# Kernel tuning notes

Measured on AMD Instinct MI355X. Metric: run time of the kernel, lower is better.

## Reference

```python
import jax, jax.numpy as jnp
import numpy as np

N = 65536        # number of encoding vectors (flattened tokens)
K = 1024         # num_embeddings (codebook size)
D = 128          # embedding_dim
BETA = 0.25


def setup_inputs() -> dict:
    key = jax.random.key(0)
    k_enc, k_cb = jax.random.split(key)
    encoding = jax.random.normal(k_enc, (N, D), dtype=jnp.float32)
    # nn.Embedding weight initialized uniform(-1/K, 1/K)
    codebook = jax.random.uniform(k_cb, (K, D), dtype=jnp.float32,
                                  minval=-1.0 / K, maxval=1.0 / K)
    return {"encoding": encoding, "codebook": codebook}


def reference(encoding, codebook):
    # Nearest codebook entry per row. argmin of L2 distance == argmin of
    # squared distance; expand ||e - w||^2 = ||e||^2 - 2 e.w + ||w||^2.
    # ||e||^2 is constant per row, so it does not affect the argmin.
    scores = (-2.0 * jnp.einsum('nd,kd->nk', encoding, codebook)
              + jnp.sum(codebook * codebook, axis=-1)[None, :])  # [N, K]
    quantized_index = jnp.argmin(scores, axis=-1)                # [N] int
    quantized_embedding = codebook[quantized_index]              # [N, D] gather == onehot @ W

    sg = jax.lax.stop_gradient
    commitment_loss = jnp.mean((sg(quantized_embedding) - encoding) ** 2)
    embedding_loss = jnp.mean((quantized_embedding - sg(encoding)) ** 2)
    vq_loss = commitment_loss * BETA + embedding_loss

    # straight-through estimator
    quantized_st = encoding + sg(quantized_embedding - encoding)

    quantized_index = quantized_index[:, None]  # match torch unsqueeze(1) -> [N, 1]
    return (quantized_index, quantized_st, vq_loss, embedding_loss, commitment_loss)
```

## Files before the change

### kernel.cpp

```cpp
#include <hip/hip_runtime.h>


#define NROWS 65536
#define KCB   1024
#define DIM   128
#define DV    32
#define MSE_DENOM 8388608.0f
#define MARGIN 3.0e-5f
#define FLAGCAP 16384
#define CSCALE   1024.0f
#define CDESCALE 0.0009765625f

#define WS_CNORM_F  256
#define WS_CN1024_F 1280
#define WS_LIST_B   12288
#define WS_PH_B     77824
#define WS_NEEDED   339968

typedef __attribute__((ext_vector_type(16))) float float16v;
typedef _Float16 half8 __attribute__((ext_vector_type(8)));
union U4H8 { uint4 u; half8 h; };
union F4A  { float4 v; float f[4]; };
union F16V { float16v v; float f[16]; };
union HU   { _Float16 f; unsigned short u; };

__device__ __forceinline__ float fmed3(float a, float b, float c) {
  return __builtin_amdgcn_fmed3f(a, b, c);
}

__global__ __launch_bounds__(64) void vq_prep0(const float* __restrict__ C,
                                               float* __restrict__ wsf) {
  int k = blockIdx.x * 64 + threadIdx.x;
  if (k == 0) { wsf[0] = 0.0f; ((unsigned*)wsf)[1] = 0u; }
  const float4* c4 = (const float4*)C + (size_t)k * DV;
  float s = 0.f;
#pragma unroll 8
  for (int i = 0; i < DV; ++i) {
    float4 v = c4[i];
    s = fmaf(v.x, v.x, s); s = fmaf(v.y, v.y, s);
    s = fmaf(v.z, v.z, s); s = fmaf(v.w, v.w, s);
  }
  wsf[WS_CNORM_F + k]  = s;
  wsf[WS_CN1024_F + k] = s * CSCALE;
}

__global__ __launch_bounds__(256) void vq_pack(const float* __restrict__ C,
                                               uint4* __restrict__ PH) {
  int g = blockIdx.x * 256 + threadIdx.x;
  int mt = g >> 9, s = (g >> 6) & 7, l = g & 63;
  int cw = mt * 32 + (l & 31);
  int k0 = s * 16 + (l >> 5) * 8;
  const float* src = C + (size_t)cw * DIM + k0;
  float4 x0 = *(const float4*)src;
  float4 x1 = *(const float4*)(src + 4);
  unsigned h[8];
  {
    float v[8] = {x0.x, x0.y, x0.z, x0.w, x1.x, x1.y, x1.z, x1.w};
#pragma unroll
    for (int j = 0; j < 8; ++j) { HU u; u.f = (_Float16)(CSCALE * v[j]); h[j] = u.u; }
  }
  PH[g] = make_uint4(h[0] | (h[1] << 16), h[2] | (h[3] << 16),
                     h[4] | (h[5] << 16), h[6] | (h[7] << 16));
}

__global__ __launch_bounds__(512, 1) void vq_main7(const float* __restrict__ E,
                                                   const float* __restrict__ C,
                                                   float* __restrict__ wsf,
                                                   float* __restrict__ out) {
  __shared__ uint4 SB[2][4096];
  __shared__ __align__(16) float CN[1024];
  __shared__ int BI[256];

  const int tid  = threadIdx.x;
  const int w    = tid >> 6;
  const int l    = tid & 63;
  const int half = l >> 5;
  const int rr   = l & 31;
  const int row0 = blockIdx.x * 256;

  const uint4* PHg = (const uint4*)((const char*)wsf + WS_PH_B);
  const uint4* CNg = (const uint4*)(wsf + WS_CN1024_F);

  uint4 stg[8];
#pragma unroll
  for (int j = 0; j < 8; ++j) stg[j] = PHg[j * 512 + tid];
  uint4 cnr;
  if (tid < 256) cnr = CNg[tid];

  half8 beh[8];
  float s2 = 0.f;
  const float* erow = E + (size_t)(row0 + w * 32 + rr) * DIM + half * 8;
#pragma unroll
  for (int s = 0; s < 8; ++s) {
    float4 x0 = *(const float4*)(erow + s * 16);
    float4 x1 = *(const float4*)(erow + s * 16 + 4);
    float v[8] = {x0.x, x0.y, x0.z, x0.w, x1.x, x1.y, x1.z, x1.w};
#pragma unroll
    for (int j = 0; j < 8; ++j) {
      float y = v[j];
      s2 = fmaf(y, y, s2);
      beh[s][j] = (_Float16)(-2.f * y);
    }
  }

#pragma unroll
  for (int j = 0; j < 8; ++j) SB[0][j * 512 + tid] = stg[j];
  if (tid < 256) ((uint4*)CN)[tid] = cnr;
  __syncthreads();

  float m1 = 3.0e38f, m2 = 3.0e38f;
  int bi0 = 0;

  for (int qt = 0; qt < 4; ++qt) {
    const int b = qt & 1;
    if (qt < 3) {
#pragma unroll
      for (int j = 0; j < 8; ++j) stg[j] = PHg[(qt + 1) * 4096 + j * 512 + tid];
    }
    const int kq = qt * 256;

#pragma unroll
    for (int tt = 0; tt < 8; ++tt) {
      const int tg = qt * 8 + tt;
      U4H8 h[8];
#pragma unroll
      for (int s = 0; s < 8; ++s) h[s].u = SB[b][tt * 512 + s * 64 + l];
      F16V acc;
#pragma unroll
      for (int q = 0; q < 4; ++q) {
        F4A c; c.v = *(const float4*)&CN[tg * 32 + q * 8 + half * 4];
        acc.f[q * 4 + 0] = c.f[0]; acc.f[q * 4 + 1] = c.f[1];
        acc.f[q * 4 + 2] = c.f[2]; acc.f[q * 4 + 3] = c.f[3];
      }
#pragma unroll
      for (int s = 0; s < 8; ++s)
        acc.v = __builtin_amdgcn_mfma_f32_32x32x16_f16(h[s].h, beh[s], acc.v, 0, 0, 0);
#pragma unroll
      for (int reg = 0; reg < 16; ++reg) {
        float sc = acc.f[reg] * CDESCALE;
        m2 = fmed3(sc, m1, m2);
        if (sc < m1) bi0 = kq + tt * 32 + (reg >> 2) * 8 + (reg & 3);
        m1 = fminf(m1, sc);
      }
    }

    if (qt < 3) {
#pragma unroll
      for (int j = 0; j < 8; ++j) SB[b ^ 1][j * 512 + tid] = stg[j];
    }
    __syncthreads();
  }

  int   bi  = bi0 + half * 4;
  float obm  = __shfl_xor(m1, 32, 64);
  float obm2 = __shfl_xor(m2, 32, 64);
  int   obi  = __shfl_xor(bi, 32, 64);
  float oen  = __shfl_xor(s2, 32, 64);
  float sv = fminf(fminf(m2, obm2), fmaxf(m1, obm));
  float bv; int bif;
  if (obm < m1 || (obm == m1 && obi < bi)) { bv = obm; bif = obi; }
  else                                     { bv = m1;  bif = bi;  }
  float en = s2 + oen;

  if (half == 0) {
    const int r = w * 32 + rr;
    out[row0 + r] = (float)bif;
    BI[r] = bif;
    if (sv - bv < MARGIN) {
      unsigned idx = atomicAdd((unsigned*)wsf + 1, 1u);
      if (idx < FLAGCAP) ((int*)((char*)wsf + WS_LIST_B))[idx] = row0 + r;
    }
    float term = en + bv;
#pragma unroll
    for (int off = 16; off > 0; off >>= 1) term += __shfl_down(term, off);
    if (rr == 0) atomicAdd(wsf, term);
  }
  __syncthreads();

  const float4* C4   = (const float4*)C;
  float4*       out4 = (float4*)out;
#pragma unroll
  for (int it = 0; it < 16; ++it) {
    int flat = it * 512 + tid;
    int r = flat >> 5, d4 = flat & 31;
    out4[(NROWS / 4) + (size_t)(row0 + r) * DV + d4] = C4[(size_t)BI[r] * DV + d4];
  }
}

__global__ __launch_bounds__(256) void vq_fix(const float* __restrict__ E,
                                              const float* __restrict__ C,
                                              float* __restrict__ wsf,
                                              float* __restrict__ out) {
  __shared__ float4 eL[4][32];
  __shared__ float  RV[4][4];
  __shared__ int    RI[4][4];
  __shared__ int    RESi[4];
  const int tid = threadIdx.x;
  const int wv  = tid >> 6;
  const int ln  = tid & 63;
  const int* list = (const int*)((const char*)wsf + WS_LIST_B);
  int nf = (int)((const unsigned*)wsf)[1];
  if (nf > FLAGCAP) nf = FLAGCAP;
  const float4* E4 = (const float4*)E;
  const float4* C4 = (const float4*)C;
  const float*  cn = wsf + WS_CNORM_F;
  float4* out4 = (float4*)out;

  for (int g = blockIdx.x; g * 4 < nf; g += gridDim.x) {
    const int base = g * 4;
    if (tid < 128) {
      int r = tid >> 5, d4 = tid & 31;
      int R = (base + r < nf) ? list[base + r] : list[base];
      eL[r][d4] = E4[(size_t)R * DV + d4];
    }
    __syncthreads();
    float bv[4] = {3.0e38f, 3.0e38f, 3.0e38f, 3.0e38f};
    int   bi[4] = {0, 0, 0, 0};
#pragma unroll
    for (int j = 0; j < 4; ++j) {
      int k = j * 256 + tid;
      float d0 = 0.f, d1 = 0.f, d2 = 0.f, d3 = 0.f;
#pragma unroll 4
      for (int d4 = 0; d4 < 32; ++d4) {
        float4 c = C4[(size_t)k * DV + d4];
        float4 e0 = eL[0][d4], e1 = eL[1][d4], e2 = eL[2][d4], e3 = eL[3][d4];
        d0 = fmaf(c.x, e0.x, d0); d0 = fmaf(c.y, e0.y, d0);
        d0 = fmaf(c.z, e0.z, d0); d0 = fmaf(c.w, e0.w, d0);
        d1 = fmaf(c.x, e1.x, d1); d1 = fmaf(c.y, e1.y, d1);
        d1 = fmaf(c.z, e1.z, d1); d1 = fmaf(c.w, e1.w, d1);
        d2 = fmaf(c.x, e2.x, d2); d2 = fmaf(c.y, e2.y, d2);
        d2 = fmaf(c.z, e2.z, d2); d2 = fmaf(c.w, e2.w, d2);
        d3 = fmaf(c.x, e3.x, d3); d3 = fmaf(c.y, e3.y, d3);
        d3 = fmaf(c.z, e3.z, d3); d3 = fmaf(c.w, e3.w, d3);
      }
      float cnk = cn[k];
      float s0 = fmaf(-2.f, d0, cnk);
      float s1 = fmaf(-2.f, d1, cnk);
      float s2 = fmaf(-2.f, d2, cnk);
      float s3 = fmaf(-2.f, d3, cnk);
      if (s0 < bv[0] || (s0 == bv[0] && k < bi[0])) { bv[0] = s0; bi[0] = k; }
      if (s1 < bv[1] || (s1 == bv[1] && k < bi[1])) { bv[1] = s1; bi[1] = k; }
      if (s2 < bv[2] || (s2 == bv[2] && k < bi[2])) { bv[2] = s2; bi[2] = k; }
      if (s3 < bv[3] || (s3 == bv[3] && k < bi[3])) { bv[3] = s3; bi[3] = k; }
    }
#pragma unroll
    for (int off = 32; off > 0; off >>= 1) {
#pragma unroll
      for (int r = 0; r < 4; ++r) {
        float wv_ = __shfl_down(bv[r], off);
        int   ji  = __shfl_down(bi[r], off);
        if (wv_ < bv[r] || (wv_ == bv[r] && ji < bi[r])) { bv[r] = wv_; bi[r] = ji; }
      }
    }
    if (ln == 0) {
#pragma unroll
      for (int r = 0; r < 4; ++r) { RV[wv][r] = bv[r]; RI[wv][r] = bi[r]; }
    }
    __syncthreads();
    if (tid < 4) {
      float v = RV[0][tid]; int i = RI[0][tid];
#pragma unroll
      for (int q = 1; q < 4; ++q) {
        float vv = RV[q][tid]; int ii = RI[q][tid];
        if (vv < v || (vv == v && ii < i)) { v = vv; i = ii; }
      }
      RESi[tid] = i;
      if (base + tid < nf) out[list[base + tid]] = (float)i;
    }
    __syncthreads();
    if (tid < 128) {
      int r = tid >> 5, d4 = tid & 31;
      if (base + r < nf) {
        int R = list[base + r];
        out4[(NROWS / 4) + (size_t)R * DV + d4] = C4[(size_t)RESi[r] * DV + d4];
      }
    }
    __syncthreads();
  }
}

__global__ void vq_final(const float* __restrict__ wsf, float* __restrict__ out) {
  if (threadIdx.x == 0 && blockIdx.x == 0) {
    float mse = wsf[0] / MSE_DENOM;
    out[NROWS + NROWS * DIM + 0] = 1.25f * mse;
    out[NROWS + NROWS * DIM + 1] = mse;
    out[NROWS + NROWS * DIM + 2] = mse;
  }
}

__global__ __launch_bounds__(256) void vq_prep_fb(const float* __restrict__ C,
                                                  float* __restrict__ ws) {
  int k = blockIdx.x * 256 + threadIdx.x;
  if (k == 0) ws[0] = 0.0f;
  const float4* c4 = (const float4*)C + (size_t)k * DV;
  float s = 0.f;
#pragma unroll 8
  for (int i = 0; i < DV; ++i) {
    float4 v = c4[i];
    s = fmaf(v.x, v.x, s); s = fmaf(v.y, v.y, s);
    s = fmaf(v.z, v.z, s); s = fmaf(v.w, v.w, s);
  }
  ws[64 + k] = s;
}

__global__ __launch_bounds__(256) void vq_main_fb(const float* __restrict__ E,
                                                  const float* __restrict__ C,
                                                  const float* __restrict__ cnorm,
                                                  float* __restrict__ out,
                                                  float* __restrict__ lossacc) {
  __shared__ float smem[16384];
  float4* EsV = (float4*)smem;
  float4* CsV = (float4*)(smem + 8192);
  const int tid  = threadIdx.x;
  const int row0 = blockIdx.x * 64;
#pragma unroll
  for (int i = 0; i < 8; ++i) {
    int flat = i * 256 + tid;
    int r = flat >> 5, d4 = flat & 31;
    EsV[r * 32 + (d4 ^ (r & 31))] = ((const float4*)E)[(size_t)(row0 + r) * DV + d4];
  }
  const int tx = tid & 15, ty = tid >> 4;
  int rbase[4], rmask[4];
#pragma unroll
  for (int i = 0; i < 4; ++i) { int r = i * 16 + ty; rbase[i] = r * 32; rmask[i] = r & 31; }
  float bestv[4]; int besti[4];
#pragma unroll
  for (int i = 0; i < 4; ++i) { bestv[i] = 3.0e38f; besti[i] = 0; }
  for (int ch = 0; ch < 16; ++ch) {
    const int k0 = ch * 64;
    __syncthreads();
#pragma unroll
    for (int i = 0; i < 8; ++i) {
      int flat = i * 256 + tid;
      int k = flat >> 5, d4 = flat & 31;
      CsV[k * 32 + (d4 ^ (k & 31))] = ((const float4*)C)[(size_t)(k0 + k) * DV + d4];
    }
    __syncthreads();
    float acc[4][4] = {};
#pragma unroll 8
    for (int d4 = 0; d4 < DV; ++d4) {
      float4 a[4], b[4];
#pragma unroll
      for (int i = 0; i < 4; ++i) a[i] = EsV[rbase[i] + (d4 ^ rmask[i])];
#pragma unroll
      for (int j = 0; j < 4; ++j) { int k = j * 16 + tx; b[j] = CsV[k * 32 + (d4 ^ (k & 31))]; }
#pragma unroll
      for (int i = 0; i < 4; ++i)
#pragma unroll
        for (int j = 0; j < 4; ++j) {
          acc[i][j] = fmaf(a[i].x, b[j].x, acc[i][j]);
          acc[i][j] = fmaf(a[i].y, b[j].y, acc[i][j]);
          acc[i][j] = fmaf(a[i].z, b[j].z, acc[i][j]);
          acc[i][j] = fmaf(a[i].w, b[j].w, acc[i][j]);
        }
    }
#pragma unroll
    for (int j = 0; j < 4; ++j) {
      int kg = k0 + j * 16 + tx;
      float cnv = cnorm[kg];
#pragma unroll
      for (int i = 0; i < 4; ++i) {
        float s = fmaf(-2.0f, acc[i][j], cnv);
        if (s < bestv[i] || (s == bestv[i] && kg < besti[i])) { bestv[i] = s; besti[i] = kg; }
      }
    }
  }
  float* Rv = smem + 8192;
  int*   Ri = (int*)(smem + 9216);
  int*   BIf = (int*)(smem + 10240);
  __syncthreads();
#pragma unroll
  for (int i = 0; i < 4; ++i) {
    int r = i * 16 + ty;
    Rv[r * 16 + tx] = bestv[i];
    Ri[r * 16 + tx] = besti[i];
  }
  __syncthreads();
  if (tid < 64) {
    const int r = tid;
    float bv = Rv[r * 16]; int bi = Ri[r * 16];
#pragma unroll
    for (int t = 1; t < 16; ++t) {
      float v = Rv[r * 16 + t]; int ii = Ri[r * 16 + t];
      if (v < bv || (v == bv && ii < bi)) { bv = v; bi = ii; }
    }
    float en = 0.f;
#pragma unroll 8
    for (int d4 = 0; d4 < DV; ++d4) {
      float4 v = EsV[r * 32 + (d4 ^ (r & 31))];
      en = fmaf(v.x, v.x, en); en = fmaf(v.y, v.y, en);
      en = fmaf(v.z, v.z, en); en = fmaf(v.w, v.w, en);
    }
    out[row0 + r] = (float)bi;
    BIf[r] = bi;
    float blocksum = en + bv;
#pragma unroll
    for (int off = 32; off > 0; off >>= 1) blocksum += __shfl_down(blocksum, off);
    if (tid == 0) atomicAdd(lossacc, blocksum);
  }
  __syncthreads();
  const float4* C4   = (const float4*)C;
  float4*       out4 = (float4*)out;
  for (int flat = tid; flat < 64 * DV; flat += 256) {
    int r = flat >> 5, d4 = flat & 31;
    out4[(NROWS / 4) + (size_t)(row0 + r) * DV + d4] = C4[(size_t)BIf[r] * DV + d4];
  }
}

__global__ void vq_final_fb(const float* __restrict__ ws, float* __restrict__ out) {
  if (threadIdx.x == 0 && blockIdx.x == 0) {
    float mse = ws[0] / MSE_DENOM;
    out[NROWS + NROWS * DIM + 0] = 1.25f * mse;
    out[NROWS + NROWS * DIM + 1] = mse;
    out[NROWS + NROWS * DIM + 2] = mse;
  }
}

extern "C" void kernel_launch(void* const* d_in, const int* in_sizes, int n_in,
                              void* d_out, int out_size, void* d_ws, size_t ws_size,
                              hipStream_t stream) {
  const float* E = (const float*)d_in[0];
  const float* C = (const float*)d_in[1];
  float* out = (float*)d_out;
  float* wsf = (float*)d_ws;

  if (ws_size >= (size_t)WS_NEEDED) {
    uint4* PH = (uint4*)((char*)d_ws + WS_PH_B);
    vq_prep0<<<16, 64, 0, stream>>>(C, wsf);
    vq_pack<<<64, 256, 0, stream>>>(C, PH);
    vq_main7<<<NROWS / 256, 512, 0, stream>>>(E, C, wsf, out);
    vq_fix<<<256, 256, 0, stream>>>(E, C, wsf, out);
    vq_final<<<1, 64, 0, stream>>>(wsf, out);
  } else {
    vq_prep_fb<<<4, 256, 0, stream>>>(C, wsf);
    vq_main_fb<<<NROWS / 64, 256, 0, stream>>>(E, C, wsf + 64, out, wsf);
    vq_final_fb<<<1, 64, 0, stream>>>(wsf, out);
  }
}
```

Before: 178.6 us.

## Split codebook across wave pairs with smaller blocks and async LDS loads

Replaces the 512-thread, 256-row main kernel with a 256-thread, 64-row kernel in which two wave pairs each scan half of the codebook, then merge their min, second-min and index through shared memory. Codebook tiles are streamed straight into LDS with global_load_lds double buffering instead of being staged in registers. Each tile's MFMA chain is split across two accumulators to shorten the dependency chain, and the descale multiply moves out of the inner loop, with the margin rescaled to match. The smaller LDS footprint allows several blocks per CU for better latency hiding, at the cost of more blocks each reloading the codebook and a larger fix-up grid.

```diff
diff --git a/kernel.cpp b/kernel.cpp
--- a/kernel.cpp
+++ b/kernel.cpp
@@ -7,6 +7,7 @@
 #define DV    32
 #define MSE_DENOM 8388608.0f
 #define MARGIN 3.0e-5f
+#define MARGINS 0.030720f
 #define FLAGCAP 16384
 #define CSCALE   1024.0f
 #define CDESCALE 0.0009765625f
@@ -26,6 +27,11 @@
 
 __device__ __forceinline__ float fmed3(float a, float b, float c) {
   return __builtin_amdgcn_fmed3f(a, b, c);
+}
+__device__ __forceinline__ void gload16(const void* g, void* s) {
+  __builtin_amdgcn_global_load_lds((const __attribute__((address_space(1))) unsigned int*)g,
+                                   (__attribute__((address_space(3))) unsigned int*)s,
+                                   16, 0, 0);
 }
 
 __global__ __launch_bounds__(64) void vq_prep0(const float* __restrict__ C,
@@ -63,33 +69,40 @@
                      h[4] | (h[5] << 16), h[6] | (h[7] << 16));
 }
 
-__global__ __launch_bounds__(512, 1) void vq_main7(const float* __restrict__ E,
+__global__ __launch_bounds__(256, 4) void vq_main8(const float* __restrict__ E,
                                                    const float* __restrict__ C,
                                                    float* __restrict__ wsf,
                                                    float* __restrict__ out) {
-  __shared__ uint4 SB[2][4096];
+  __shared__ uint4 SH[2][1024];
   __shared__ __align__(16) float CN[1024];
-  __shared__ int BI[256];
+  __shared__ float X1[64], X2[64];
+  __shared__ int   XI[64];
+  __shared__ int   BI[64];
 
   const int tid  = threadIdx.x;
   const int w    = tid >> 6;
   const int l    = tid & 63;
   const int half = l >> 5;
   const int rr   = l & 31;
-  const int row0 = blockIdx.x * 256;
+  const int pair = w >> 1;
+  const int rw   = w & 1;
+  const int row0 = blockIdx.x * 64;
+  const int row  = row0 + rw * 32 + rr;
 
   const uint4* PHg = (const uint4*)((const char*)wsf + WS_PH_B);
-  const uint4* CNg = (const uint4*)(wsf + WS_CN1024_F);
-
-  uint4 stg[8];
-#pragma unroll
-  for (int j = 0; j < 8; ++j) stg[j] = PHg[j * 512 + tid];
-  uint4 cnr;
-  if (tid < 256) cnr = CNg[tid];
+
+  {
+    uint4* base = &SH[0][0];
+    gload16(PHg + tid,                  base + tid);
+    gload16(PHg + 256 + tid,            base + 256 + tid);
+    gload16(PHg + 16 * 512 + tid,       base + 512 + tid);
+    gload16(PHg + 16 * 512 + 256 + tid, base + 768 + tid);
+    gload16(((const uint4*)(wsf + WS_CN1024_F)) + tid, ((uint4*)CN) + tid);
+  }
 
   half8 beh[8];
   float s2 = 0.f;
-  const float* erow = E + (size_t)(row0 + w * 32 + rr) * DIM + half * 8;
+  const float* erow = E + (size_t)row * DIM + half * 8;
 #pragma unroll
   for (int s = 0; s < 8; ++s) {
     float4 x0 = *(const float4*)(erow + s * 16);
@@ -103,74 +116,84 @@
     }
   }
 
-#pragma unroll
-  for (int j = 0; j < 8; ++j) SB[0][j * 512 + tid] = stg[j];
-  if (tid < 256) ((uint4*)CN)[tid] = cnr;
+  asm volatile("s_waitcnt vmcnt(0)" ::: "memory");
   __syncthreads();
 
   float m1 = 3.0e38f, m2 = 3.0e38f;
-  int bi0 = 0;
-
-  for (int qt = 0; qt < 4; ++qt) {
-    const int b = qt & 1;
-    if (qt < 3) {
-#pragma unroll
-      for (int j = 0; j < 8; ++j) stg[j] = PHg[(qt + 1) * 4096 + j * 512 + tid];
-    }
-    const int kq = qt * 256;
-
-#pragma unroll
-    for (int tt = 0; tt < 8; ++tt) {
-      const int tg = qt * 8 + tt;
-      U4H8 h[8];
-#pragma unroll
-      for (int s = 0; s < 8; ++s) h[s].u = SB[b][tt * 512 + s * 64 + l];
-      F16V acc;
-#pragma unroll
-      for (int q = 0; q < 4; ++q) {
-        F4A c; c.v = *(const float4*)&CN[tg * 32 + q * 8 + half * 4];
-        acc.f[q * 4 + 0] = c.f[0]; acc.f[q * 4 + 1] = c.f[1];
-        acc.f[q * 4 + 2] = c.f[2]; acc.f[q * 4 + 3] = c.f[3];
-      }
-#pragma unroll
-      for (int s = 0; s < 8; ++s)
-        acc.v = __builtin_amdgcn_mfma_f32_32x32x16_f16(h[s].h, beh[s], acc.v, 0, 0, 0);
-#pragma unroll
-      for (int reg = 0; reg < 16; ++reg) {
-        float sc = acc.f[reg] * CDESCALE;
-        m2 = fmed3(sc, m1, m2);
-        if (sc < m1) bi0 = kq + tt * 32 + (reg >> 2) * 8 + (reg & 3);
-        m1 = fminf(m1, sc);
-      }
-    }
-
-    if (qt < 3) {
-#pragma unroll
-      for (int j = 0; j < 8; ++j) SB[b ^ 1][j * 512 + tid] = stg[j];
-    }
-    __syncthreads();
-  }
-
-  int   bi  = bi0 + half * 4;
-  float obm  = __shfl_xor(m1, 32, 64);
-  float obm2 = __shfl_xor(m2, 32, 64);
-  int   obi  = __shfl_xor(bi, 32, 64);
-  float oen  = __shfl_xor(s2, 32, 64);
-  float sv = fminf(fminf(m2, obm2), fmaxf(m1, obm));
-  float bv; int bif;
-  if (obm < m1 || (obm == m1 && obi < bi)) { bv = obm; bif = obi; }
-  else                                     { bv = m1;  bif = bi;  }
-  float en = s2 + oen;
-
-  if (half == 0) {
-    const int r = w * 32 + rr;
-    out[row0 + r] = (float)bif;
-    BI[r] = bif;
-    if (sv - bv < MARGIN) {
+  int   bi = 0;
+
+  for (int st = 0; st < 16; ++st) {
+    const int buf = st & 1;
+    const int tg  = pair * 16 + st;
+    if (st < 15) {
+      uint4* nb = &SH[buf ^ 1][0];
+      const uint4* s0 = PHg + (size_t)(st + 1) * 512;
+      const uint4* s1 = PHg + (size_t)(17 + st) * 512;
+      gload16(s0 + tid,       nb + tid);
+      gload16(s0 + 256 + tid, nb + 256 + tid);
+      gload16(s1 + tid,       nb + 512 + tid);
+      gload16(s1 + 256 + tid, nb + 768 + tid);
+    }
+
+    F16V accA, accB;
+#pragma unroll
+    for (int q = 0; q < 4; ++q) {
+      F4A c; c.v = *(const float4*)&CN[tg * 32 + q * 8 + half * 4];
+      accA.f[q * 4 + 0] = c.f[0]; accA.f[q * 4 + 1] = c.f[1];
+      accA.f[q * 4 + 2] = c.f[2]; accA.f[q * 4 + 3] = c.f[3];
+    }
+    accB.v = (float16v){0,0,0,0,0,0,0,0,0,0,0,0,0,0,0,0};
+#pragma unroll
+    for (int s = 0; s < 8; s += 2) {
+      U4H8 h0, h1;
+      h0.u = SH[buf][pair * 512 + s * 64 + l];
+      h1.u = SH[buf][pair * 512 + (s + 1) * 64 + l];
+      accA.v = __builtin_amdgcn_mfma_f32_32x32x16_f16(h0.h, beh[s],     accA.v, 0, 0, 0);
+      accB.v = __builtin_amdgcn_mfma_f32_32x32x16_f16(h1.h, beh[s + 1], accB.v, 0, 0, 0);
+    }
+
+    const int kb = tg * 32 + half * 4;
+#pragma unroll
+    for (int reg = 0; reg < 16; ++reg) {
+      float sc = accA.f[reg] + accB.f[reg];
+      bool nb_ = sc < m1;
+      m2 = fmed3(sc, m1, m2);
+      m1 = fminf(sc, m1);
+      bi = nb_ ? (kb + (reg >> 2) * 8 + (reg & 3)) : bi;
+    }
+
+    asm volatile("s_waitcnt vmcnt(0)" ::: "memory");
+    __syncthreads();
+  }
+
+  {
+    float om1 = __shfl_xor(m1, 32, 64);
+    float om2 = __shfl_xor(m2, 32, 64);
+    int   obi = __shfl_xor(bi, 32, 64);
+    float nsv = fminf(fminf(m2, om2), fmaxf(m1, om1));
+    if (om1 < m1 || (om1 == m1 && obi < bi)) { m1 = om1; bi = obi; }
+    m2 = nsv;
+  }
+  float en = s2 + __shfl_xor(s2, 32, 64);
+
+  if (pair == 1 && half == 0) {
+    X1[rw * 32 + rr] = m1; X2[rw * 32 + rr] = m2; XI[rw * 32 + rr] = bi;
+  }
+  __syncthreads();
+
+  if (pair == 0 && half == 0) {
+    const int r = rw * 32 + rr;
+    float xb = X1[r], xs = X2[r];
+    int   xi = XI[r];
+    float sv = fminf(fminf(m2, xs), fmaxf(m1, xb));
+    if (xb < m1 || (xb == m1 && xi < bi)) { m1 = xb; bi = xi; }
+    out[row] = (float)bi;
+    BI[r] = bi;
+    if (sv - m1 < MARGINS) {
       unsigned idx = atomicAdd((unsigned*)wsf + 1, 1u);
-      if (idx < FLAGCAP) ((int*)((char*)wsf + WS_LIST_B))[idx] = row0 + r;
-    }
-    float term = en + bv;
+      if (idx < FLAGCAP) ((int*)((char*)wsf + WS_LIST_B))[idx] = row;
+    }
+    float term = fmaf(m1, CDESCALE, en);
 #pragma unroll
     for (int off = 16; off > 0; off >>= 1) term += __shfl_down(term, off);
     if (rr == 0) atomicAdd(wsf, term);
@@ -180,8 +203,8 @@
   const float4* C4   = (const float4*)C;
   float4*       out4 = (float4*)out;
 #pragma unroll
-  for (int it = 0; it < 16; ++it) {
-    int flat = it * 512 + tid;
+  for (int it = 0; it < 8; ++it) {
+    int flat = it * 256 + tid;
     int r = flat >> 5, d4 = flat & 31;
     out4[(NROWS / 4) + (size_t)(row0 + r) * DV + d4] = C4[(size_t)BI[r] * DV + d4];
   }
@@ -428,8 +451,8 @@
     uint4* PH = (uint4*)((char*)d_ws + WS_PH_B);
     vq_prep0<<<16, 64, 0, stream>>>(C, wsf);
     vq_pack<<<64, 256, 0, stream>>>(C, PH);
-    vq_main7<<<NROWS / 256, 512, 0, stream>>>(E, C, wsf, out);
-    vq_fix<<<256, 256, 0, stream>>>(E, C, wsf, out);
+    vq_main8<<<NROWS / 64, 256, 0, stream>>>(E, C, wsf, out);
+    vq_fix<<<512, 256, 0, stream>>>(E, C, wsf, out);
     vq_final<<<1, 64, 0, stream>>>(wsf, out);
   } else {
     vq_prep_fb<<<4, 256, 0, stream>>>(C, wsf);
```

Measured after the change: 161.0 us. 1.11x faster.

## Stage codebook directly into LDS and split MFMA accumulator chains

Applied to the files above, without the earlier changes.

Codebook tiles and norms are now copied with global_load_lds straight into shared memory, with no register staging, followed by an explicit vmcnt wait before each barrier. The MFMA chain is split into two independent accumulators, and the argmin tracking into two interleaved min/second-min streams. This is meant to cut the serial dependency latency and the per-score rescale multiply, since the descale is now folded into the margin and the loss term. The fix-up kernel gets twice as many blocks. The risk is that the rescaled margin changes how many rows are flagged for exact recheck.

```diff
diff --git a/kernel.cpp b/kernel.cpp
--- a/kernel.cpp
+++ b/kernel.cpp
@@ -7,6 +7,7 @@
 #define DV    32
 #define MSE_DENOM 8388608.0f
 #define MARGIN 3.0e-5f
+#define MARGINS 0.030720f
 #define FLAGCAP 16384
 #define CSCALE   1024.0f
 #define CDESCALE 0.0009765625f
@@ -26,6 +27,11 @@
 
 __device__ __forceinline__ float fmed3(float a, float b, float c) {
   return __builtin_amdgcn_fmed3f(a, b, c);
+}
+__device__ __forceinline__ void gload16(const void* g, void* s) {
+  __builtin_amdgcn_global_load_lds((const __attribute__((address_space(1))) unsigned int*)g,
+                                   (__attribute__((address_space(3))) unsigned int*)s,
+                                   16, 0, 0);
 }
 
 __global__ __launch_bounds__(64) void vq_prep0(const float* __restrict__ C,
@@ -63,7 +69,7 @@
                      h[4] | (h[5] << 16), h[6] | (h[7] << 16));
 }
 
-__global__ __launch_bounds__(512, 1) void vq_main7(const float* __restrict__ E,
+__global__ __launch_bounds__(512, 1) void vq_main9(const float* __restrict__ E,
                                                    const float* __restrict__ C,
                                                    float* __restrict__ wsf,
                                                    float* __restrict__ out) {
@@ -81,11 +87,10 @@
   const uint4* PHg = (const uint4*)((const char*)wsf + WS_PH_B);
   const uint4* CNg = (const uint4*)(wsf + WS_CN1024_F);
 
-  uint4 stg[8];
-#pragma unroll
-  for (int j = 0; j < 8; ++j) stg[j] = PHg[j * 512 + tid];
-  uint4 cnr;
-  if (tid < 256) cnr = CNg[tid];
+#pragma unroll
+  for (int j = 0; j < 8; ++j)
+    gload16(PHg + j * 512 + tid, &SB[0][0] + j * 512 + tid);
+  if (tid < 256) gload16(CNg + tid, ((uint4*)CN) + tid);
 
   half8 beh[8];
   float s2 = 0.f;
@@ -103,21 +108,20 @@
     }
   }
 
-#pragma unroll
-  for (int j = 0; j < 8; ++j) SB[0][j * 512 + tid] = stg[j];
-  if (tid < 256) ((uint4*)CN)[tid] = cnr;
+  asm volatile("s_waitcnt vmcnt(0)" ::: "memory");
   __syncthreads();
 
-  float m1 = 3.0e38f, m2 = 3.0e38f;
-  int bi0 = 0;
+  float m1a = 3.0e38f, m2a = 3.0e38f, m1b = 3.0e38f, m2b = 3.0e38f;
+  int bia = 0, bib = 0;
 
   for (int qt = 0; qt < 4; ++qt) {
     const int b = qt & 1;
     if (qt < 3) {
 #pragma unroll
-      for (int j = 0; j < 8; ++j) stg[j] = PHg[(qt + 1) * 4096 + j * 512 + tid];
-    }
-    const int kq = qt * 256;
+      for (int j = 0; j < 8; ++j)
+        gload16(PHg + (qt + 1) * 4096 + j * 512 + tid,
+                &SB[b ^ 1][0] + j * 512 + tid);
+    }
 
 #pragma unroll
     for (int tt = 0; tt < 8; ++tt) {
@@ -125,52 +129,71 @@
       U4H8 h[8];
 #pragma unroll
       for (int s = 0; s < 8; ++s) h[s].u = SB[b][tt * 512 + s * 64 + l];
-      F16V acc;
+
+      F16V accA, accB;
 #pragma unroll
       for (int q = 0; q < 4; ++q) {
         F4A c; c.v = *(const float4*)&CN[tg * 32 + q * 8 + half * 4];
-        acc.f[q * 4 + 0] = c.f[0]; acc.f[q * 4 + 1] = c.f[1];
-        acc.f[q * 4 + 2] = c.f[2]; acc.f[q * 4 + 3] = c.f[3];
-      }
-#pragma unroll
-      for (int s = 0; s < 8; ++s)
-        acc.v = __builtin_amdgcn_mfma_f32_32x32x16_f16(h[s].h, beh[s], acc.v, 0, 0, 0);
-#pragma unroll
-      for (int reg = 0; reg < 16; ++reg) {
-        float sc = acc.f[reg] * CDESCALE;
-        m2 = fmed3(sc, m1, m2);
-        if (sc < m1) bi0 = kq + tt * 32 + (reg >> 2) * 8 + (reg & 3);
-        m1 = fminf(m1, sc);
-      }
-    }
-
-    if (qt < 3) {
-#pragma unroll
-      for (int j = 0; j < 8; ++j) SB[b ^ 1][j * 512 + tid] = stg[j];
-    }
-    __syncthreads();
-  }
-
-  int   bi  = bi0 + half * 4;
-  float obm  = __shfl_xor(m1, 32, 64);
-  float obm2 = __shfl_xor(m2, 32, 64);
-  int   obi  = __shfl_xor(bi, 32, 64);
-  float oen  = __shfl_xor(s2, 32, 64);
-  float sv = fminf(fminf(m2, obm2), fmaxf(m1, obm));
-  float bv; int bif;
-  if (obm < m1 || (obm == m1 && obi < bi)) { bv = obm; bif = obi; }
-  else                                     { bv = m1;  bif = bi;  }
-  float en = s2 + oen;
+        accA.f[q * 4 + 0] = c.f[0]; accA.f[q * 4 + 1] = c.f[1];
+        accA.f[q * 4 + 2] = c.f[2]; accA.f[q * 4 + 3] = c.f[3];
+      }
+      accB.v = (float16v){0,0,0,0,0,0,0,0,0,0,0,0,0,0,0,0};
+#pragma unroll
+      for (int s = 0; s < 8; s += 2) {
+        accA.v = __builtin_amdgcn_mfma_f32_32x32x16_f16(h[s].h,     beh[s],     accA.v, 0, 0, 0);
+        accB.v = __builtin_amdgcn_mfma_f32_32x32x16_f16(h[s + 1].h, beh[s + 1], accB.v, 0, 0, 0);
+      }
+
+      const int kb = tg * 32 + half * 4;
+#pragma unroll
+      for (int reg = 0; reg < 16; reg += 2) {
+        {
+          float sc = accA.f[reg] + accB.f[reg];
+          bool nb_ = sc < m1a;
+          m2a = fmed3(sc, m1a, m2a);
+          m1a = fminf(sc, m1a);
+          bia = nb_ ? (kb + (reg >> 2) * 8 + (reg & 3)) : bia;
+        }
+        {
+          float sc = accA.f[reg + 1] + accB.f[reg + 1];
+          bool nb_ = sc < m1b;
+          m2b = fmed3(sc, m1b, m2b);
+          m1b = fminf(sc, m1b);
+          bib = nb_ ? (kb + ((reg + 1) >> 2) * 8 + ((reg + 1) & 3)) : bib;
+        }
+      }
+    }
+
+    asm volatile("s_waitcnt vmcnt(0)" ::: "memory");
+    __syncthreads();
+  }
+
+  float m1, m2; int bi;
+  {
+    m2 = fminf(fminf(m2a, m2b), fmaxf(m1a, m1b));
+    if (m1b < m1a || (m1b == m1a && bib < bia)) { m1 = m1b; bi = bib; }
+    else                                        { m1 = m1a; bi = bia; }
+  }
+
+  {
+    float om1 = __shfl_xor(m1, 32, 64);
+    float om2 = __shfl_xor(m2, 32, 64);
+    int   obi = __shfl_xor(bi, 32, 64);
+    float nsv = fminf(fminf(m2, om2), fmaxf(m1, om1));
+    if (om1 < m1 || (om1 == m1 && obi < bi)) { m1 = om1; bi = obi; }
+    m2 = nsv;
+  }
+  float en = s2 + __shfl_xor(s2, 32, 64);
 
   if (half == 0) {
     const int r = w * 32 + rr;
-    out[row0 + r] = (float)bif;
-    BI[r] = bif;
-    if (sv - bv < MARGIN) {
+    out[row0 + r] = (float)bi;
+    BI[r] = bi;
+    if (m2 - m1 < MARGINS) {
       unsigned idx = atomicAdd((unsigned*)wsf + 1, 1u);
       if (idx < FLAGCAP) ((int*)((char*)wsf + WS_LIST_B))[idx] = row0 + r;
     }
-    float term = en + bv;
+    float term = fmaf(m1, CDESCALE, en);
 #pragma unroll
     for (int off = 16; off > 0; off >>= 1) term += __shfl_down(term, off);
     if (rr == 0) atomicAdd(wsf, term);
@@ -428,8 +451,8 @@
     uint4* PH = (uint4*)((char*)d_ws + WS_PH_B);
     vq_prep0<<<16, 64, 0, stream>>>(C, wsf);
     vq_pack<<<64, 256, 0, stream>>>(C, PH);
-    vq_main7<<<NROWS / 256, 512, 0, stream>>>(E, C, wsf, out);
-    vq_fix<<<256, 256, 0, stream>>>(E, C, wsf, out);
+    vq_main9<<<NROWS / 256, 512, 0, stream>>>(E, C, wsf, out);
+    vq_fix<<<512, 256, 0, stream>>>(E, C, wsf, out);
     vq_final<<<1, 64, 0, stream>>>(wsf, out);
   } else {
     vq_prep_fb<<<4, 256, 0, stream>>>(C, wsf);
```

New measurement: 165.0 us. 7.6% less time.
